# Optimization experiments

Measured on AMD Instinct MI355X. Metric: run time of the kernel, lower is better.

Reference implementation:

```python
import jax, jax.numpy as jnp
import numpy as np

BLANK = 0
NEG = -1e30  # safe -inf surrogate for log-domain DP


def _ctc_loss_mean(pred, label, label_length):
    # pred: [B, T, C] raw logits; label: [B, Lmax] int; label_length: [B] int
    B, T, C = pred.shape
    Lmax = label.shape[1]
    S = 2 * Lmax + 1

    logp = jax.nn.log_softmax(pred.astype(jnp.float32), axis=-1)  # [B, T, C]

    # extended label sequence: blank, l1, blank, l2, ..., blank  -> [B, S]
    ext = jnp.full((B, S), BLANK, dtype=label.dtype)
    ext = ext.at[:, 1::2].set(label)
    prev2 = jnp.pad(ext[:, :-2], ((0, 0), (2, 0)), constant_values=BLANK)
    skip = (ext != BLANK) & (ext != prev2) & (jnp.arange(S) >= 2)  # [B, S]

    # gather log-probs of extended labels per time step: [T, B, S]
    lp = jnp.transpose(logp, (1, 0, 2))  # [T, B, C]
    lp_ext = jnp.take_along_axis(
        lp, jnp.broadcast_to(ext[None].astype(jnp.int32), (T, B, S)), axis=2)

    # alpha recursion (forward DP in log space)
    alpha0 = jnp.full((B, S), NEG, dtype=jnp.float32)
    alpha0 = alpha0.at[:, 0].set(lp_ext[0, :, 0])
    alpha0 = alpha0.at[:, 1].set(lp_ext[0, :, 1])

    def step(alpha, lp_t):
        s1 = jnp.pad(alpha[:, :-1], ((0, 0), (1, 0)), constant_values=NEG)
        s2 = jnp.pad(alpha[:, :-2], ((0, 0), (2, 0)), constant_values=NEG)
        a = jnp.logaddexp(alpha, s1)
        a = jnp.where(skip, jnp.logaddexp(a, s2), a)
        return a + lp_t, None

    alpha, _ = jax.lax.scan(step, alpha0, lp_ext[1:])  # [B, S]

    # total log-likelihood: last blank (s=2L) or last label (s=2L-1)
    L = label_length.astype(jnp.int32)
    a_last = jnp.take_along_axis(alpha, (2 * L)[:, None], axis=1)[:, 0]
    a_prev = jnp.take_along_axis(alpha, (2 * L - 1)[:, None], axis=1)[:, 0]
    loss = -jnp.logaddexp(a_last, a_prev)  # [B]

    # torch CTCLoss(reduction='mean'): mean over batch of loss / target_length
    return jnp.mean(loss / L.astype(jnp.float32))


def setup_inputs() -> dict:
    key = jax.random.key(0)
    k1, k2, k3 = jax.random.split(key, 3)
    B, T, C, Lmax = 128, 128, 6625, 25
    pred = jax.random.normal(k1, (B, T, C), dtype=jnp.float32)
    label = jax.random.randint(k2, (B, Lmax), 1, C, dtype=jnp.int32)
    label_length = jax.random.randint(k3, (B,), 1, Lmax + 1, dtype=jnp.int32)
    return {"pred": pred, "label": label, "label_length": label_length}


def reference(pred, label, label_length):
    return _ctc_loss_mean(pred, label, label_length)
```

## Files before the change

kernel.cpp:

```cpp
#include <hip/hip_runtime.h>
#include <hip/hip_bf16.h>

#define NEGINF (-1e30f)

constexpr int Bsz  = 128;
constexpr int Tlen = 128;
constexpr int Ccls = 6625;
constexpr int Lmax = 25;
constexpr int Sext = 2 * Lmax + 1;

__global__ __launch_bounds__(256, 8) void lse_gather_kernel(
        const float* __restrict__ pred,
        const int*   __restrict__ label,
        float*       __restrict__ lp_ext,
        float*       __restrict__ out) {
    const int bt  = blockIdx.x;
    const int tid = threadIdx.x;

    const size_t row_start = (size_t)bt * Ccls;
    const size_t w0   = row_start & ~(size_t)3;
    const int    lead = (int)(row_start - w0);
    const float4* win = (const float4*)(pred + w0);

    float gval = 0.0f;
    if (tid < Sext) {
        int b = bt >> 7;
        int cls = (tid & 1) ? label[b * Lmax + (tid >> 1)] : 0;
        gval = pred[row_start + cls];
    }

    float4 v[7];
    #pragma unroll
    for (int it = 0; it < 6; ++it) v[it] = win[tid + it * 256];
    if (tid < 121) v[6] = win[tid + 6 * 256];
    else           v[6] = make_float4(NEGINF, NEGINF, NEGINF, NEGINF);

    const int ebase0 = tid * 4 - lead;
    float s0 = 0.f, s1 = 0.f, s2 = 0.f, s3 = 0.f;
    #pragma unroll
    for (int it = 0; it < 7; ++it) {
        int e = ebase0 + it * 1024;
        float x0 = ((unsigned)(e + 0) < (unsigned)Ccls) ? v[it].x : NEGINF;
        float x1 = ((unsigned)(e + 1) < (unsigned)Ccls) ? v[it].y : NEGINF;
        float x2 = ((unsigned)(e + 2) < (unsigned)Ccls) ? v[it].z : NEGINF;
        float x3 = ((unsigned)(e + 3) < (unsigned)Ccls) ? v[it].w : NEGINF;
        s0 += __expf(x0);
        s1 += __expf(x1);
        s2 += __expf(x2);
        s3 += __expf(x3);
    }
    float s = (s0 + s1) + (s2 + s3);

    #pragma unroll
    for (int off = 32; off > 0; off >>= 1) s += __shfl_xor(s, off);
    __shared__ float red[4];
    const int wave = tid >> 6, lane = tid & 63;
    if (lane == 0) red[wave] = s;
    __syncthreads();
    const float Sv = (red[0] + red[1]) + (red[2] + red[3]);

    if (tid < Sext)
        lp_ext[(size_t)bt * Sext + tid] = gval - __logf(Sv);

    if (bt == 0 && tid == 0) out[0] = 0.0f;
}

__global__ __launch_bounds__(128) void ctc_dp_kernel(
        const float* __restrict__ lp_ext,
        const int*   __restrict__ label,
        const int*   __restrict__ lablen,
        float*       __restrict__ out) {
    const int b   = blockIdx.x;
    const int tid = threadIdx.x;

    __shared__ float lp[Tlen * Sext];
    const float4* src4 = (const float4*)(lp_ext + (size_t)b * Tlen * Sext);
    float4* dst4 = (float4*)lp;
    constexpr int N4 = (Tlen * Sext) / 4;
    #pragma unroll
    for (int it = 0; it < (N4 + 127) / 128; ++it) {
        int i = tid + it * 128;
        if (i < N4) dst4[i] = src4[i];
    }
    __syncthreads();

    if (tid < 64) {
        const int lane = tid;

        bool skip = false;
        if ((lane & 1) && lane >= 3 && lane < Sext) {
            int k = lane >> 1;
            skip = (label[b * Lmax + k] != label[b * Lmax + k - 1]);
        }
        const bool live = (lane < Sext);

        float alpha = NEGINF;
        if (live && lane <= 1) alpha = lp[lane];

        #pragma unroll 4
        for (int t = 1; t < Tlen; ++t) {
            float lpt = live ? lp[t * Sext + lane] : NEGINF;
            float s1 = __shfl_up(alpha, 1);
            float s2 = __shfl_up(alpha, 2);
            if (lane < 1) s1 = NEGINF;
            if (!skip)    s2 = NEGINF;
            float M = fmaxf(fmaxf(alpha, s1), s2);
            float sum = __expf(alpha - M) + __expf(s1 - M) + __expf(s2 - M);
            alpha = M + __logf(sum) + lpt;
        }

        int L = lablen[b];
        float a = __shfl(alpha, 2 * L);
        float p = __shfl(alpha, 2 * L - 1);
        if (lane == 0) {
            float M = fmaxf(a, p);
            float ll = M + __logf(__expf(a - M) + __expf(p - M));
            atomicAdd(out, -ll / (float)L * (1.0f / (float)Bsz));
        }
    }
}

extern "C" void kernel_launch(void* const* d_in, const int* in_sizes, int n_in,
                              void* d_out, int out_size, void* d_ws, size_t ws_size,
                              hipStream_t stream) {
    const float* pred   = (const float*)d_in[0];
    const int*   label  = (const int*)d_in[1];
    const int*   lablen = (const int*)d_in[2];
    float* out = (float*)d_out;

    float* lp_ext = (float*)d_ws;

    lse_gather_kernel<<<Bsz * Tlen, 256, 0, stream>>>(pred, label, lp_ext, out);
    ctc_dp_kernel<<<Bsz, 128, 0, stream>>>(lp_ext, label, lablen, out);
}
```

Before: 96.44 us.

## Map one wavefront per row in LSE kernel, removing block reduction

Each 64-lane wavefront now computes the log-sum-exp of a whole row, so one block of 256 threads covers four rows and the launch uses a quarter as many blocks. The shared-memory reduction and __syncthreads go away, and the boundary masking is applied only on the first and last iterations. In exchange each lane issues 26 sequential float4 loads instead of 7, which could lower memory-level parallelism per lane unless the unrolled loads are kept in flight together.

```diff
diff --git a/kernel.cpp b/kernel.cpp
--- a/kernel.cpp
+++ b/kernel.cpp
@@ -14,55 +14,54 @@
         const int*   __restrict__ label,
         float*       __restrict__ lp_ext,
         float*       __restrict__ out) {
-    const int bt  = blockIdx.x;
-    const int tid = threadIdx.x;
+    const int tid  = threadIdx.x;
+    const int wave = tid >> 6, lane = tid & 63;
+    const int row  = blockIdx.x * 4 + wave;
 
-    const size_t row_start = (size_t)bt * Ccls;
+    const size_t row_start = (size_t)row * Ccls;
     const size_t w0   = row_start & ~(size_t)3;
     const int    lead = (int)(row_start - w0);
     const float4* win = (const float4*)(pred + w0);
 
     float gval = 0.0f;
-    if (tid < Sext) {
-        int b = bt >> 7;
-        int cls = (tid & 1) ? label[b * Lmax + (tid >> 1)] : 0;
+    if (lane < Sext) {
+        int b   = row >> 7;
+        int cls = (lane & 1) ? label[b * Lmax + (lane >> 1)] : 0;
         gval = pred[row_start + cls];
     }
 
-    float4 v[7];
-    #pragma unroll
-    for (int it = 0; it < 6; ++it) v[it] = win[tid + it * 256];
-    if (tid < 121) v[6] = win[tid + 6 * 256];
-    else           v[6] = make_float4(NEGINF, NEGINF, NEGINF, NEGINF);
-
-    const int ebase0 = tid * 4 - lead;
     float s0 = 0.f, s1 = 0.f, s2 = 0.f, s3 = 0.f;
     #pragma unroll
-    for (int it = 0; it < 7; ++it) {
-        int e = ebase0 + it * 1024;
-        float x0 = ((unsigned)(e + 0) < (unsigned)Ccls) ? v[it].x : NEGINF;
-        float x1 = ((unsigned)(e + 1) < (unsigned)Ccls) ? v[it].y : NEGINF;
-        float x2 = ((unsigned)(e + 2) < (unsigned)Ccls) ? v[it].z : NEGINF;
-        float x3 = ((unsigned)(e + 3) < (unsigned)Ccls) ? v[it].w : NEGINF;
-        s0 += __expf(x0);
-        s1 += __expf(x1);
-        s2 += __expf(x2);
-        s3 += __expf(x3);
+    for (int it = 0; it < 26; ++it) {
+        const int idx = lane + it * 64;
+        float4 x;
+        if (it < 25) {
+            x = win[idx];
+        } else {
+            if (lane < 57) x = win[idx];
+            else           x = make_float4(NEGINF, NEGINF, NEGINF, NEGINF);
+        }
+        if (it == 0 || it == 25) {
+            const int e = idx * 4 - lead;
+            x.x = ((unsigned)(e + 0) < (unsigned)Ccls) ? x.x : NEGINF;
+            x.y = ((unsigned)(e + 1) < (unsigned)Ccls) ? x.y : NEGINF;
+            x.z = ((unsigned)(e + 2) < (unsigned)Ccls) ? x.z : NEGINF;
+            x.w = ((unsigned)(e + 3) < (unsigned)Ccls) ? x.w : NEGINF;
+        }
+        s0 += __expf(x.x);
+        s1 += __expf(x.y);
+        s2 += __expf(x.z);
+        s3 += __expf(x.w);
     }
     float s = (s0 + s1) + (s2 + s3);
 
     #pragma unroll
     for (int off = 32; off > 0; off >>= 1) s += __shfl_xor(s, off);
-    __shared__ float red[4];
-    const int wave = tid >> 6, lane = tid & 63;
-    if (lane == 0) red[wave] = s;
-    __syncthreads();
-    const float Sv = (red[0] + red[1]) + (red[2] + red[3]);
 
-    if (tid < Sext)
-        lp_ext[(size_t)bt * Sext + tid] = gval - __logf(Sv);
+    if (lane < Sext)
+        lp_ext[(size_t)row * Sext + lane] = gval - __logf(s);
 
-    if (bt == 0 && tid == 0) out[0] = 0.0f;
+    if (blockIdx.x == 0 && tid == 0) out[0] = 0.0f;
 }
 
 __global__ __launch_bounds__(128) void ctc_dp_kernel(
@@ -130,6 +129,6 @@
 
     float* lp_ext = (float*)d_ws;
 
-    lse_gather_kernel<<<Bsz * Tlen, 256, 0, stream>>>(pred, label, lp_ext, out);
+    lse_gather_kernel<<<(Bsz * Tlen) / 4, 256, 0, stream>>>(pred, label, lp_ext, out);
     ctc_dp_kernel<<<Bsz, 128, 0, stream>>>(lp_ext, label, lablen, out);
 }
```

Measured after the change: 169.9 us. +76.2%, slower.
